# Kernel tuning notes

Measured on AMD Instinct MI355X. Metric: run time of the kernel, lower is better.

The kernel has to match this reference:

```python
import jax, jax.numpy as jnp
import numpy as np

B, N_UNK, M_KNOWN = 8, 8192, 2048
C1, C2 = 256, 256
MLP = [512, 256, 256]
K_ENC = 32
D = MLP[-1]


def setup_inputs() -> dict:
    key = jax.random.key(0)
    ks = jax.random.split(key, 16)
    return {
        "unknown": jax.random.normal(ks[0], (B, N_UNK, 3), jnp.float32),
        "known": jax.random.normal(ks[1], (B, M_KNOWN, 3), jnp.float32),
        "unknow_feats": jax.random.normal(ks[2], (B, C1, N_UNK), jnp.float32),
        "known_feats": jax.random.normal(ks[3], (B, C2, M_KNOWN), jnp.float32),
        "conv_w1": jax.random.normal(ks[4], (MLP[1], MLP[0]), jnp.float32) * 0.05,
        "conv_b1": jnp.zeros((MLP[1],), jnp.float32),
        "bn_g1": jnp.ones((MLP[1],), jnp.float32),
        "bn_b1": jnp.zeros((MLP[1],), jnp.float32),
        "bn_m1": jax.random.normal(ks[5], (MLP[1],), jnp.float32) * 0.01,
        "bn_v1": jax.random.uniform(ks[6], (MLP[1],), jnp.float32, 0.5, 1.5),
        "conv_w2": jax.random.normal(ks[7], (MLP[2], MLP[1]), jnp.float32) * 0.05,
        "conv_b2": jnp.zeros((MLP[2],), jnp.float32),
        "bn_g2": jnp.ones((MLP[2],), jnp.float32),
        "bn_b2": jnp.zeros((MLP[2],), jnp.float32),
        "bn_m2": jax.random.normal(ks[8], (MLP[2],), jnp.float32) * 0.01,
        "bn_v2": jax.random.uniform(ks[9], (MLP[2],), jnp.float32, 0.5, 1.5),
        "enc_codewords": jax.random.normal(ks[10], (K_ENC, D), jnp.float32) * float(1.0 / np.sqrt(K_ENC * D)),
        "enc_scale": jax.random.uniform(ks[11], (K_ENC,), jnp.float32, -1.0, 0.0),
        "lin_w": jax.random.normal(ks[12], (D, D * K_ENC), jnp.float32) * 0.02,
        "lin_b": jnp.zeros((D,), jnp.float32),
    }


def _conv_bn_relu(x, w, b, g, beta, mean, var):
    # 1x1 conv over (B,C,N) == channel GEMM, then BN (inference form), then ReLU
    x = jnp.einsum("oc,bcn->bon", w, x) + b[None, :, None]
    x = g[None, :, None] * (x - mean[None, :, None]) * jax.lax.rsqrt(var + 1e-5)[None, :, None] + beta[None, :, None]
    return jax.nn.relu(x)


def reference(unknown, known, unknow_feats, known_feats,
              conv_w1, conv_b1, bn_g1, bn_b1, bn_m1, bn_v1,
              conv_w2, conv_b2, bn_g2, bn_b2, bn_m2, bn_v2,
              enc_codewords, enc_scale, lin_w, lin_b):
    # ---- three_nn: 3 nearest known points for each unknown point ----
    x2 = jnp.sum(unknown * unknown, axis=-1)            # (B,n)
    y2 = jnp.sum(known * known, axis=-1)                # (B,m)
    d2 = x2[:, :, None] - 2.0 * jnp.einsum("bnc,bmc->bnm", unknown, known) + y2[:, None, :]
    dist = jnp.sqrt(jnp.maximum(d2, 1e-12))             # (B,n,m) Euclidean
    neg_d, idx = jax.lax.top_k(-dist, 3)                # 3 smallest
    dist3 = -neg_d                                      # (B,n,3)
    dist_recip = 1.0 / (dist3 + 1e-8)
    weight = dist_recip / jnp.sum(dist_recip, axis=2, keepdims=True)
    # ---- three_interpolate: gather + weighted sum ----
    gathered = jax.vmap(lambda f, i: f[:, i])(known_feats, idx)   # (B,C2,n,3)
    interp = jnp.einsum("bcnk,bnk->bcn", gathered, weight)        # (B,C2,n)
    feats = jnp.concatenate([interp, unknow_feats], axis=1)       # (B,C2+C1,n)
    # ---- SharedMLP (two 1x1 conv + BN + ReLU layers) ----
    h = _conv_bn_relu(feats, conv_w1, conv_b1, bn_g1, bn_b1, bn_m1, bn_v1)
    h = _conv_bn_relu(h, conv_w2, conv_b2, bn_g2, bn_b2, bn_m2, bn_v2)   # (B,D,n)
    # ---- Encoding layer (soft dictionary assignment, residual aggregate) ----
    X = jnp.swapaxes(h, 1, 2)                                     # (B,n,D)
    c2 = jnp.sum(enc_codewords * enc_codewords, axis=-1)          # (K,)
    xn2 = jnp.sum(X * X, axis=-1)                                 # (B,n)
    # scaled_l2: s_k * ||x - c_k||^2 without materializing (B,n,K,D) residuals
    sl = enc_scale[None, None, :] * (xn2[:, :, None] - 2.0 * jnp.einsum("bnd,kd->bnk", X, enc_codewords) + c2[None, None, :])
    A = jax.nn.softmax(sl, axis=-1)                               # (B,n,K)
    E = jnp.einsum("bnk,bnd->bkd", A, X) - jnp.sum(A, axis=1)[:, :, None] * enc_codewords[None]
    E = jax.nn.relu(E).reshape(E.shape[0], -1)                    # (B,K*D)
    E = E / jnp.maximum(jnp.linalg.norm(E, axis=1, keepdims=True), 1e-12)  # F.normalize
    ctx = jax.nn.sigmoid(E @ lin_w.T + lin_b)                     # (B,D)
    # ---- channel-attention fusion ----
    return h * ctx[:, :, None]                                    # (B,D,n)
```

## Files before the change

kernel.cpp:

```cpp
#include <hip/hip_runtime.h>
#include <stdint.h>

typedef unsigned short u16;
typedef unsigned int u32;
typedef __attribute__((ext_vector_type(8))) short short8;
typedef __attribute__((ext_vector_type(4))) float f32x4;
typedef __attribute__((ext_vector_type(4))) u32 u32x4;

#define B_ 8
#define N_ 8192
#define M_ 2048
#define DD 256
#define KENC 32

#define SC1 0
#define SH1 256
#define SC2 512
#define SH2 768
#define C2OFF 1024
#define SOFF 1056
#define RNOFF 1088

#define OFF_IDX3   0ull
#define OFF_W3     786432ull
#define OFF_FT     1572864ull
#define OFF_H1T    68681728ull
#define OFF_ERELU  102236160ull
#define OFF_PART   102498304ull
#define OFF_CONSTS 102760448ull
#define OFF_CTX    102768640ull
#define OFF_W1D    102776832ull
#define OFF_W2D    103038976ull
#define OFF_CWD    103170048ull
#define OFF_FLAG   103186432ull

__device__ __forceinline__ float bf2f(u16 v){ return __uint_as_float(((u32)v)<<16); }
__device__ __forceinline__ u16 f2bf(float f){
  u32 x = __float_as_uint(f);
  return (u16)((x + 0x7FFFu + ((x>>16)&1u)) >> 16);
}
__device__ __forceinline__ float ldf(const void* p, size_t i, int f){
  return f ? ((const float*)p)[i] : bf2f(((const u16*)p)[i]);
}
__device__ __forceinline__ void gl_lds16(const u16* g, u16* l){
  __builtin_amdgcn_global_load_lds(
      (const __attribute__((address_space(1))) void*)g,
      (__attribute__((address_space(3))) void*)l, 16, 0, 0);
}

__global__ __launch_bounds__(256) void k_detect(const void* v1, int* flagp){
  __shared__ int cntb, cntf;
  int t = threadIdx.x;
  if (t==0){ cntb=0; cntf=0; }
  __syncthreads();
  float vb = bf2f(((const u16*)v1)[t]);
  if (!(vb > 0.4f && vb < 1.6f)) atomicAdd(&cntb, 1);
  if (t < 64){
    float vf = ((const float*)v1)[t];
    if (!(vf > 0.4f && vf < 1.6f)) atomicAdd(&cntf, 1);
  }
  __syncthreads();
  if (t==0) flagp[0] = (cntb > 0 && cntf == 0) ? 1 : 0;
}

__global__ __launch_bounds__(256) void k_convert(
    const void* w1, const void* w2, const void* cwsrc, const int* __restrict__ flagp,
    u16* __restrict__ W1d, u16* __restrict__ W2d, u16* __restrict__ CWd){
  int id = blockIdx.x*256 + threadIdx.x;
  int f = flagp[0];
  if (id < 131072){
    W1d[id] = f ? f2bf(((const float*)w1)[id]) : ((const u16*)w1)[id];
  } else if (id < 196608){
    int j = id - 131072;
    W2d[j] = f ? f2bf(((const float*)w2)[j]) : ((const u16*)w2)[j];
  } else if (id < 204800){
    int j = id - 196608;
    CWd[j] = f ? f2bf(((const float*)cwsrc)[j]) : ((const u16*)cwsrc)[j];
  }
}

__global__ __launch_bounds__(256) void k0_setup(
    const void* cb1, const void* g1, const void* be1, const void* m1, const void* v1,
    const void* cb2, const void* g2, const void* be2, const void* m2, const void* v2,
    const u16* __restrict__ CWd, const void* es, const int* __restrict__ flagp,
    float* __restrict__ consts){
  int t = threadIdx.x;
  int f = flagp[0];
  {
    float g = ldf(g1,t,f), be = ldf(be1,t,f), m = ldf(m1,t,f), v = ldf(v1,t,f), cb = ldf(cb1,t,f);
    float r = 1.f/sqrtf(v + 1e-5f);
    float sc = g*r;
    consts[SC1+t] = sc; consts[SH1+t] = (cb-m)*sc + be;
  }
  {
    float g = ldf(g2,t,f), be = ldf(be2,t,f), m = ldf(m2,t,f), v = ldf(v2,t,f), cb = ldf(cb2,t,f);
    float r = 1.f/sqrtf(v + 1e-5f);
    float sc = g*r;
    consts[SC2+t] = sc; consts[SH2+t] = (cb-m)*sc + be;
  }
  if (t < KENC){
    float s = 0.f;
    for (int d=0; d<DD; d++){ float c = bf2f(CWd[t*DD+d]); s = fmaf(c,c,s); }
    consts[C2OFF+t] = s;
    consts[SOFF+t]  = ldf(es,t,f);
  }
}

__global__ __launch_bounds__(256) void k1_three_nn(
    const void* unknown, const void* known, const int* __restrict__ flagp,
    int* __restrict__ idx3, float* __restrict__ w3){
  __shared__ float4 kp[M_];
  int b = blockIdx.y, t = threadIdx.x;
  int f = flagp[0];
  for (int i=t; i<M_; i+=256){
    size_t o = ((size_t)b*M_ + i)*3;
    float x = ldf(known,o,f), y = ldf(known,o+1,f), z = ldf(known,o+2,f);
    float y2 = __fadd_rn(__fadd_rn(__fmul_rn(x,x), __fmul_rn(y,y)), __fmul_rn(z,z));
    kp[i] = make_float4(x,y,z,y2);
  }
  __syncthreads();
  int qq = t >> 3, sl = t & 7;
  int pid = blockIdx.x*32 + qq;
  size_t uo = ((size_t)b*N_ + pid)*3;
  float ux=ldf(unknown,uo,f), uy=ldf(unknown,uo+1,f), uz=ldf(unknown,uo+2,f);
  float x2 = __fadd_rn(__fadd_rn(__fmul_rn(ux,ux), __fmul_rn(uy,uy)), __fmul_rn(uz,uz));
  float u2x = ux+ux, u2y = uy+uy, u2z = uz+uz;
  float b0=3.4e38f, b1=3.4e38f, b2v=3.4e38f;
  int i0=-1, i1=-1, i2=-1;
  for (int j0=0; j0<256; j0+=4){
    float d[4]; int mi[4];
    #pragma unroll
    for (int u=0; u<4; u++){
      int m = (j0+u)*8 + sl;
      mi[u] = m;
      float4 km = kp[m];
      float dot2 = __fadd_rn(__fadd_rn(__fmul_rn(u2x,km.x), __fmul_rn(u2y,km.y)), __fmul_rn(u2z,km.z));
      d[u] = __fadd_rn(__fsub_rn(x2, dot2), km.w);
    }
    #pragma unroll
    for (int u=0; u<4; u++){
      float d2 = d[u];
      if (__builtin_expect(d2 < b2v, 0)){
        int m = mi[u];
        bool lt0 = d2 < b0, lt1 = d2 < b1;
        b2v = lt1 ? b1 : d2;                     i2 = lt1 ? i1 : m;
        float nb1 = lt0 ? b0 : (lt1 ? d2 : b1);  int ni1 = lt0 ? i0 : (lt1 ? m : i1);
        b0  = lt0 ? d2 : b0;                     i0 = lt0 ? m : i0;
        b1 = nb1; i1 = ni1;
      }
    }
  }
  #pragma unroll
  for (int st=1; st<8; st<<=1){
    float o0=__shfl_xor(b0,st,64), o1=__shfl_xor(b1,st,64), o2=__shfl_xor(b2v,st,64);
    int   j0=__shfl_xor(i0,st,64), j1=__shfl_xor(i1,st,64), j2=__shfl_xor(i2,st,64);
    float dv[3] = {o0,o1,o2}; int jv[3] = {j0,j1,j2};
    #pragma unroll
    for (int e=0; e<3; e++){
      float dd = dv[e]; int jj = jv[e];
      bool lt2 = (dd < b2v) || (dd == b2v && jj < i2);
      if (lt2){
        bool lt0 = (dd < b0) || (dd == b0 && jj < i0);
        bool lt1 = (dd < b1) || (dd == b1 && jj < i1);
        if (lt0){ b2v=b1;i2=i1; b1=b0;i1=i0; b0=dd;i0=jj; }
        else if (lt1){ b2v=b1;i2=i1; b1=dd;i1=jj; }
        else { b2v=dd; i2=jj; }
      }
    }
  }
  if (sl == 0){
    float da = __fsqrt_rn(fmaxf(b0,1e-12f));
    float db = __fsqrt_rn(fmaxf(b1,1e-12f));
    float dc = __fsqrt_rn(fmaxf(b2v,1e-12f));
    float r0 = __fdiv_rn(1.f, __fadd_rn(da,1e-8f));
    float r1 = __fdiv_rn(1.f, __fadd_rn(db,1e-8f));
    float r2 = __fdiv_rn(1.f, __fadd_rn(dc,1e-8f));
    float rs = __fadd_rn(__fadd_rn(r0,r1),r2);
    size_t o = ((size_t)b*N_ + pid)*3;
    idx3[o]=i0; idx3[o+1]=i1; idx3[o+2]=i2;
    w3[o]=__fdiv_rn(r0,rs); w3[o+1]=__fdiv_rn(r1,rs); w3[o+2]=__fdiv_rn(r2,rs);
  }
}

__global__ __launch_bounds__(256) void k2_interp(
    const void* kf, const int* __restrict__ idx3,
    const float* __restrict__ w3, const int* __restrict__ flagp, u16* __restrict__ Ft){
  __shared__ u16 Ls[M_*8];
  int ct = blockIdx.x;
  int rg = blockIdx.y;
  int b = blockIdx.z, t = threadIdx.x;
  int f = flagp[0];
  for (int cp=0; cp<4; cp++){
    int c0 = ct*8 + cp*2;
    size_t base0 = ((size_t)b*DD + c0)*M_;
    size_t base1 = base0 + M_;
    for (int i=t; i<M_; i+=256){
      float f0 = ldf(kf, base0+i, f);
      float f1 = ldf(kf, base1+i, f);
      u32 w = (u32)f2bf(f0) | ((u32)f2bf(f1)<<16);
      *(u32*)(Ls + i*8 + cp*2) = w;
    }
  }
  __syncthreads();
  for (int rep=rg*8; rep<rg*8+8; rep++){
    int pid = rep*256 + t;
    size_t o3 = ((size_t)b*N_ + pid)*3;
    int ia = idx3[o3], ib = idx3[o3+1], ic = idx3[o3+2];
    float wa = w3[o3], wb = w3[o3+1], wc = w3[o3+2];
    short8 va = *(const short8*)(Ls + ia*8);
    short8 vb = *(const short8*)(Ls + ib*8);
    short8 vc = *(const short8*)(Ls + ic*8);
    u32x4 pk;
    #pragma unroll
    for (int cq=0; cq<4; cq++){
      float fa0 = bf2f((u16)va[cq*2]),   fb0 = bf2f((u16)vb[cq*2]),   fc0 = bf2f((u16)vc[cq*2]);
      float fa1 = bf2f((u16)va[cq*2+1]), fb1 = bf2f((u16)vb[cq*2+1]), fc1 = bf2f((u16)vc[cq*2+1]);
      float v0 = fmaf(wc, fc0, fmaf(wb, fb0, wa*fa0));
      float v1 = fmaf(wc, fc1, fmaf(wb, fb1, wa*fa1));
      pk[cq] = (u32)f2bf(v0) | ((u32)f2bf(v1)<<16);
    }
    *(u32x4*)(Ft + ((size_t)b*N_ + pid)*512 + ct*8) = pk;
  }
}

__global__ __launch_bounds__(256) void k2b_transpose_uf(
    const void* uf, const int* __restrict__ flagp, u16* __restrict__ Ft){
  __shared__ u16 Ls[64*72];
  int bx = blockIdx.x, cy = blockIdx.y, b = blockIdx.z, t = threadIdx.x;
  int f = flagp[0];
  {
    int n = t & 63, cg = t >> 6;
    for (int i=0; i<16; i++){
      int c = cg*16 + i;
      Ls[n*72 + c] = f2bf(ldf(uf, ((size_t)b*DD + cy*64 + c)*N_ + bx*64 + n, f));
    }
  }
  __syncthreads();
  int nl = t>>2, cc = t&3;
  u16* dst = Ft + ((size_t)b*N_ + bx*64 + nl)*512 + 256 + cy*64 + cc*16;
  *(u32x4*)dst     = *(const u32x4*)(Ls + nl*72 + cc*16);
  *(u32x4*)(dst+8) = *(const u32x4*)(Ls + nl*72 + cc*16 + 8);
}

__global__ __launch_bounds__(256) void gemm_bn_relu(
    const u16* __restrict__ W, const u16* __restrict__ Fin,
    const float* __restrict__ consts, int sc_off, int sh_off,
    u16* __restrict__ Out, int K){
  __shared__ u16 SM[17408];
  u16* As = SM; u16* Bs = SM + 8192;
  int b = blockIdx.z, ot = blockIdx.y*128, nt = blockIdx.x*128;
  int t = threadIdx.x, wave = t>>6, lane = t&63, ln = lane&15, quad = lane>>4;
  int wo = (wave&1)*64, wn = (wave>>1)*64;
  f32x4 acc[4][4];
  #pragma unroll
  for (int i=0;i<4;i++)
    #pragma unroll
    for (int j=0;j<4;j++) acc[i][j] = (f32x4)0.f;
  const u16* Wp = W + (size_t)ot*K;
  const u16* Fp = Fin + ((size_t)b*N_ + nt)*K;
  for (int kk=0; kk<K; kk+=64){
    #pragma unroll
    for (int i=0;i<4;i++){
      int c = wave*256 + i*64 + lane;
      int r = c>>3, k8 = (c&7) ^ (r&7);
      const u16* gA = Wp + (size_t)r*K + kk + k8*8;
      const u16* gB = Fp + (size_t)r*K + kk + k8*8;
      gl_lds16(gA, As + (size_t)(wave*256 + i*64)*8);
      gl_lds16(gB, Bs + (size_t)(wave*256 + i*64)*8);
    }
    __syncthreads();
    #pragma unroll
    for (int kh=0; kh<2; kh++){
      short8 af[4], bfr[4];
      #pragma unroll
      for (int i=0;i<4;i++){
        int R = wo + i*16 + ln, C = kh*4 + quad;
        af[i] = *(const short8*)(As + (size_t)(R*8 + (C^(R&7)))*8);
      }
      #pragma unroll
      for (int j=0;j<4;j++){
        int R = wn + j*16 + ln, C = kh*4 + quad;
        bfr[j] = *(const short8*)(Bs + (size_t)(R*8 + (C^(R&7)))*8);
      }
      #pragma unroll
      for (int i=0;i<4;i++)
        #pragma unroll
        for (int j=0;j<4;j++)
          acc[i][j] = __builtin_amdgcn_mfma_f32_16x16x32_bf16(af[i], bfr[j], acc[i][j], 0,0,0);
    }
    __syncthreads();
  }
  u16* Cs = SM;
  #pragma unroll
  for (int i=0;i<4;i++){
    #pragma unroll
    for (int r=0;r<4;r++){
      int ol = wo + i*16 + quad*4 + r;
      float sc = consts[sc_off + ot + ol], sh = consts[sh_off + ot + ol];
      #pragma unroll
      for (int j=0;j<4;j++){
        float v = fmaxf(fmaf(acc[i][j][r], sc, sh), 0.f);
        Cs[(wn + j*16 + ln)*136 + ol] = f2bf(v);
      }
    }
  }
  __syncthreads();
  int nl = t>>1, half = t&1;
  u16* dst = Out + ((size_t)b*N_ + nt + nl)*256 + ot + half*64;
  const u16* srcr = Cs + nl*136 + half*64;
  #pragma unroll
  for (int c=0;c<8;c++)
    *(u32x4*)(dst + c*8) = *(const u32x4*)(srcr + c*8);
}

__global__ __launch_bounds__(256) void k5_enc_partial(
    const u16* __restrict__ X, const u16* __restrict__ cw,
    const float* __restrict__ consts, float* __restrict__ Epart){
  __shared__ u16 Xs[64*264];
  __shared__ float A_lds[64*32];
  __shared__ float xn2s[64];
  int g = blockIdx.x, b = blockIdx.y, t = threadIdx.x;
  int wave = t>>6, lane = t&63, ln = lane&15, quad = lane>>4;
  int ka = lane>>1, h = lane&1;
  int dbase = wave*64 + h*32;
  float accE[32];
  #pragma unroll
  for (int p=0;p<32;p++) accE[p]=0.f;
  float asum = 0.f;
  float c2v0 = consts[C2OFF + ln], c2v1 = consts[C2OFF + 16 + ln];
  float sv0  = consts[SOFF + ln],  sv1  = consts[SOFF + 16 + ln];
  for (int tt=0; tt<2; tt++){
    int n0 = (g*2+tt)*64;
    const u16* Xp = X + ((size_t)b*N_ + n0)*256;
    #pragma unroll
    for (int i=0;i<8;i++){
      int ch = t + i*256;
      int r = ch>>5, kc = (ch&31)*8;
      *(u32x4*)(Xs + r*264 + kc) = *(const u32x4*)(Xp + r*256 + kc);
    }
    __syncthreads();
    {
      int row = t>>2, part = t&3;
      const u16* rp = Xs + row*264 + part*64;
      float s = 0.f;
      #pragma unroll
      for (int d=0; d<64; d+=8){
        short8 xv = *(const short8*)(rp + d);
        #pragma unroll
        for (int q=0;q<8;q++){ float x = bf2f((u16)xv[q]); s = fmaf(x,x,s); }
      }
      s += __shfl_xor(s,1,64);
      s += __shfl_xor(s,2,64);
      if (part==0) xn2s[row] = s;
    }
    __syncthreads();
    f32x4 pj0 = (f32x4)0.f, pj1 = (f32x4)0.f;
    const u16* xrow = Xs + (wave*16 + ln)*264;
    #pragma unroll
    for (int kk=0; kk<256; kk+=32){
      short8 a   = *(const short8*)(xrow + kk + quad*8);
      short8 bf0 = *(const short8*)(cw + (size_t)ln*256 + kk + quad*8);
      short8 bf1 = *(const short8*)(cw + (size_t)(16+ln)*256 + kk + quad*8);
      pj0 = __builtin_amdgcn_mfma_f32_16x16x32_bf16(a, bf0, pj0, 0,0,0);
      pj1 = __builtin_amdgcn_mfma_f32_16x16x32_bf16(a, bf1, pj1, 0,0,0);
    }
    #pragma unroll
    for (int r=0;r<4;r++){
      int nl = wave*16 + quad*4 + r;
      float xv = xn2s[nl];
      float v0 = sv0 * __fadd_rn(__fsub_rn(xv, __fmul_rn(2.f,pj0[r])), c2v0);
      float v1 = sv1 * __fadd_rn(__fsub_rn(xv, __fmul_rn(2.f,pj1[r])), c2v1);
      float mx = fmaxf(v0,v1);
      #pragma unroll
      for (int d=1; d<16; d<<=1) mx = fmaxf(mx, __shfl_xor(mx, d, 64));
      float e0 = __expf(v0-mx), e1 = __expf(v1-mx);
      float es = e0+e1;
      #pragma unroll
      for (int d=1; d<16; d<<=1) es += __shfl_xor(es, d, 64);
      float inv = 1.f/es;
      A_lds[nl*32 + ln]      = e0*inv;
      A_lds[nl*32 + 16 + ln] = e1*inv;
    }
    __syncthreads();
    #pragma unroll 2
    for (int n=0; n<64; n++){
      float a = A_lds[n*32 + ka];
      asum += a;
      const u16* xr = Xs + n*264 + dbase;
      #pragma unroll
      for (int p8=0; p8<4; p8++){
        u32x4 xv = *(const u32x4*)(xr + p8*8);
        #pragma unroll
        for (int q=0; q<4; q++){
          u32 w = xv[q];
          float lo = __uint_as_float(w<<16);
          float hi = __uint_as_float(w & 0xffff0000u);
          accE[p8*8 + q*2]   = fmaf(a, lo, accE[p8*8 + q*2]);
          accE[p8*8 + q*2+1] = fmaf(a, hi, accE[p8*8 + q*2+1]);
        }
      }
    }
    __syncthreads();
  }
  int slab = b*64 + g;
  float* Ed = Epart + (size_t)slab*8224 + (size_t)ka*257 + dbase;
  #pragma unroll
  for (int p=0;p<32;p++) Ed[p] = accE[p];
  if (t < 64 && h == 0) Epart[(size_t)slab*8224 + (size_t)ka*257 + 256] = asum;
}

__global__ __launch_bounds__(256) void k5b_reduce(
    const float* __restrict__ Epart, const u16* __restrict__ cw, float* __restrict__ Erelu){
  int id = blockIdx.x*256 + threadIdx.x;
  int d = id & 255, k = (id>>8)&31, b = id>>13;
  float s = 0.f, as = 0.f;
  for (int sl=0; sl<64; sl++){
    const float* Ep = Epart + ((size_t)(b*64+sl))*8224 + (size_t)k*257;
    s  += Ep[d];
    as += Ep[256];
  }
  float cv = bf2f(cw[k*256+d]);
  Erelu[(size_t)b*8192 + k*256 + d] = fmaxf(s - as*cv, 0.f);
}

__global__ __launch_bounds__(256) void k6a_norm(
    const float* __restrict__ Erelu, float* __restrict__ consts){
  __shared__ float red[256];
  int b = blockIdx.x, t = threadIdx.x;
  float s = 0.f;
  for (int i=0;i<32;i++){ float e = Erelu[(size_t)b*8192 + i*256 + t]; s = fmaf(e,e,s); }
  red[t] = s; __syncthreads();
  for (int w=128; w>0; w>>=1){ if (t<w) red[t] += red[t+w]; __syncthreads(); }
  if (t==0) consts[RNOFF + b] = 1.f/fmaxf(__fsqrt_rn(red[0]), 1e-12f);
}

__global__ __launch_bounds__(256) void k6b_partial(
    const float* __restrict__ Erelu, const void* lw, const int* __restrict__ flagp,
    float* __restrict__ partials){
  __shared__ float Er[256];
  int kc = blockIdx.x, b = blockIdx.y, t = threadIdx.x;
  int f = flagp[0];
  Er[t] = Erelu[(size_t)b*8192 + kc*256 + t];
  __syncthreads();
  float s = 0.f;
  if (f){
    const float* lwp = (const float*)lw + (size_t)t*8192 + kc*256;
    for (int p=0; p<256; p+=4){
      f32x4 v = *(const f32x4*)(lwp + p);
      #pragma unroll
      for (int q=0;q<4;q++) s = fmaf(Er[p+q], v[q], s);
    }
  } else {
    const u16* lwp = (const u16*)lw + (size_t)t*8192 + kc*256;
    for (int p=0; p<256; p+=8){
      u32x4 v = *(const u32x4*)(lwp + p);
      #pragma unroll
      for (int q=0;q<4;q++){
        u32 w = v[q];
        s = fmaf(Er[p+q*2],   __uint_as_float(w<<16), s);
        s = fmaf(Er[p+q*2+1], __uint_as_float(w & 0xffff0000u), s);
      }
    }
  }
  partials[((size_t)b*32 + kc)*256 + t] = s;
}

__global__ __launch_bounds__(256) void k6c_ctx(
    const float* __restrict__ partials, const float* __restrict__ consts,
    const void* lb, const int* __restrict__ flagp, float* __restrict__ ctx){
  int b = blockIdx.x, t = threadIdx.x;
  int f = flagp[0];
  float s = 0.f;
  for (int kc=0; kc<32; kc++) s += partials[((size_t)b*32+kc)*256 + t];
  float x = fmaf(consts[RNOFF+b], s, ldf(lb,t,f));
  ctx[b*256 + t] = 1.f/(1.f + __expf(-x));
}

__global__ __launch_bounds__(256) void k7_out(
    const u16* __restrict__ ht, const float* __restrict__ ctx,
    const int* __restrict__ flagp, void* out){
  __shared__ u16 Ls[64*72];
  int bx = blockIdx.x, oy = blockIdx.y, b = blockIdx.z, t = threadIdx.x;
  int f = flagp[0];
  {
    int nl = t>>2, oc = t&3;
    const u16* src = ht + ((size_t)b*N_ + bx*64 + nl)*256 + oy*64 + oc*16;
    *(u32x4*)(Ls + nl*72 + oc*16)     = *(const u32x4*)src;
    *(u32x4*)(Ls + nl*72 + oc*16 + 8) = *(const u32x4*)(src + 8);
  }
  __syncthreads();
  int ol = t>>2, nc = t&3;
  float cv = ctx[b*256 + oy*64 + ol];
  size_t dstoff = ((size_t)b*DD + oy*64 + ol)*N_ + bx*64 + nc*16;
  if (f){
    float* dst = (float*)out + dstoff;
    #pragma unroll
    for (int wq=0; wq<4; wq++){
      f32x4 v;
      #pragma unroll
      for (int q=0;q<4;q++) v[q] = bf2f(Ls[(nc*16 + wq*4 + q)*72 + ol]) * cv;
      *(f32x4*)(dst + wq*4) = v;
    }
  } else {
    u32 words[8];
    #pragma unroll
    for (int wq=0; wq<8; wq++){
      float v0 = bf2f(Ls[(nc*16 + wq*2)*72 + ol]) * cv;
      float v1 = bf2f(Ls[(nc*16 + wq*2+1)*72 + ol]) * cv;
      words[wq] = (u32)f2bf(v0) | ((u32)f2bf(v1)<<16);
    }
    u16* dst = (u16*)out + dstoff;
    u32x4 w0 = {words[0],words[1],words[2],words[3]};
    u32x4 w1 = {words[4],words[5],words[6],words[7]};
    *(u32x4*)dst     = w0;
    *(u32x4*)(dst+8) = w1;
  }
}

extern "C" void kernel_launch(void* const* d_in, const int* in_sizes, int n_in,
                              void* d_out, int out_size, void* d_ws, size_t ws_size,
                              hipStream_t stream){
  const void* unknown = d_in[0];
  const void* known   = d_in[1];
  const void* uf      = d_in[2];
  const void* kf      = d_in[3];
  const void* w1      = d_in[4];
  const void* cb1     = d_in[5];
  const void* g1      = d_in[6];
  const void* be1     = d_in[7];
  const void* m1      = d_in[8];
  const void* v1      = d_in[9];
  const void* w2      = d_in[10];
  const void* cb2     = d_in[11];
  const void* g2      = d_in[12];
  const void* be2     = d_in[13];
  const void* m2      = d_in[14];
  const void* v2      = d_in[15];
  const void* cw      = d_in[16];
  const void* es      = d_in[17];
  const void* lw      = d_in[18];
  const void* lb      = d_in[19];

  char* ws = (char*)d_ws;
  int*   idx3  = (int*)(ws + OFF_IDX3);
  float* w3    = (float*)(ws + OFF_W3);
  u16*   Ft    = (u16*)(ws + OFF_FT);
  u16*   ht    = Ft;
  u16*   h1t   = (u16*)(ws + OFF_H1T);
  float* Epart = (float*)(ws + OFF_H1T);
  float* Erelu    = (float*)(ws + OFF_ERELU);
  float* partials = (float*)(ws + OFF_PART);
  float* consts   = (float*)(ws + OFF_CONSTS);
  float* ctx      = (float*)(ws + OFF_CTX);
  u16*   W1d   = (u16*)(ws + OFF_W1D);
  u16*   W2d   = (u16*)(ws + OFF_W2D);
  u16*   CWd   = (u16*)(ws + OFF_CWD);
  int*   flagp = (int*)(ws + OFF_FLAG);

  k_detect<<<1, 256, 0, stream>>>(v1, flagp);
  k_convert<<<800, 256, 0, stream>>>(w1, w2, cw, flagp, W1d, W2d, CWd);
  k0_setup<<<1, 256, 0, stream>>>(cb1,g1,be1,m1,v1, cb2,g2,be2,m2,v2, CWd, es, flagp, consts);
  k1_three_nn<<<dim3(256,8), 256, 0, stream>>>(unknown, known, flagp, idx3, w3);
  k2_interp<<<dim3(32,4,8), 256, 0, stream>>>(kf, idx3, w3, flagp, Ft);
  k2b_transpose_uf<<<dim3(128,4,8), 256, 0, stream>>>(uf, flagp, Ft);
  gemm_bn_relu<<<dim3(64,2,8), 256, 0, stream>>>(W1d, Ft,  consts, SC1, SH1, h1t, 512);
  gemm_bn_relu<<<dim3(64,2,8), 256, 0, stream>>>(W2d, h1t, consts, SC2, SH2, ht,  256);
  k5_enc_partial<<<dim3(64,8), 256, 0, stream>>>(ht, CWd, consts, Epart);
  k5b_reduce<<<256, 256, 0, stream>>>(Epart, CWd, Erelu);
  k6a_norm<<<8, 256, 0, stream>>>(Erelu, consts);
  k6b_partial<<<dim3(32,8), 256, 0, stream>>>(Erelu, lw, flagp, partials);
  k6c_ctx<<<8, 256, 0, stream>>>(partials, consts, lb, flagp, ctx);
  k7_out<<<dim3(128,4,8), 256, 0, stream>>>(ht, ctx, flagp, d_out);
}
```

Baseline: 458.8 us.

## Rebalance three_nn lanes and split encoding partials into more swizzled blocks

The three_nn kernel now assigns 4 lanes per query instead of 8, so each block handles 64 queries and the grid is halved, with each lane scanning twice as many known points. The encoding partial kernel processes one 64-row tile per block instead of two, doubling the grid to 128 slabs per batch. It replaces padded LDS rows with an XOR swizzle, keeps row norms in registers and shuffles them instead of staging through LDS, and adds an occupancy hint. Asum moves to a separate buffer. The aim is better occupancy and fewer bank conflicts, at the cost of twice as many partial slabs for the reduce kernel to read.

```diff
diff --git a/kernel.cpp b/kernel.cpp
--- a/kernel.cpp
+++ b/kernel.cpp
@@ -119,19 +119,19 @@
     kp[i] = make_float4(x,y,z,y2);
   }
   __syncthreads();
-  int qq = t >> 3, sl = t & 7;
-  int pid = blockIdx.x*32 + qq;
+  int qq = t >> 2, sl = t & 3;
+  int pid = blockIdx.x*64 + qq;
   size_t uo = ((size_t)b*N_ + pid)*3;
   float ux=ldf(unknown,uo,f), uy=ldf(unknown,uo+1,f), uz=ldf(unknown,uo+2,f);
   float x2 = __fadd_rn(__fadd_rn(__fmul_rn(ux,ux), __fmul_rn(uy,uy)), __fmul_rn(uz,uz));
   float u2x = ux+ux, u2y = uy+uy, u2z = uz+uz;
   float b0=3.4e38f, b1=3.4e38f, b2v=3.4e38f;
   int i0=-1, i1=-1, i2=-1;
-  for (int j0=0; j0<256; j0+=4){
+  for (int j0=0; j0<512; j0+=4){
     float d[4]; int mi[4];
     #pragma unroll
     for (int u=0; u<4; u++){
-      int m = (j0+u)*8 + sl;
+      int m = (j0+u)*4 + sl;
       mi[u] = m;
       float4 km = kp[m];
       float dot2 = __fadd_rn(__fadd_rn(__fmul_rn(u2x,km.x), __fmul_rn(u2y,km.y)), __fmul_rn(u2z,km.z));
@@ -151,7 +151,7 @@
     }
   }
   #pragma unroll
-  for (int st=1; st<8; st<<=1){
+  for (int st=1; st<4; st<<=1){
     float o0=__shfl_xor(b0,st,64), o1=__shfl_xor(b1,st,64), o2=__shfl_xor(b2v,st,64);
     int   j0=__shfl_xor(i0,st,64), j1=__shfl_xor(i1,st,64), j2=__shfl_xor(i2,st,64);
     float dv[3] = {o0,o1,o2}; int jv[3] = {j0,j1,j2};
@@ -313,111 +313,113 @@
     *(u32x4*)(dst + c*8) = *(const u32x4*)(srcr + c*8);
 }
 
-__global__ __launch_bounds__(256) void k5_enc_partial(
+__global__ __launch_bounds__(256, 6) void k5_enc_partial(
     const u16* __restrict__ X, const u16* __restrict__ cw,
-    const float* __restrict__ consts, float* __restrict__ Epart){
-  __shared__ u16 Xs[64*264];
+    const float* __restrict__ consts, float* __restrict__ Epart,
+    float* __restrict__ Asum){
+  __shared__ u16 Xs[64*256];
   __shared__ float A_lds[64*32];
-  __shared__ float xn2s[64];
   int g = blockIdx.x, b = blockIdx.y, t = threadIdx.x;
   int wave = t>>6, lane = t&63, ln = lane&15, quad = lane>>4;
   int ka = lane>>1, h = lane&1;
   int dbase = wave*64 + h*32;
-  float accE[32];
-  #pragma unroll
-  for (int p=0;p<32;p++) accE[p]=0.f;
-  float asum = 0.f;
   float c2v0 = consts[C2OFF + ln], c2v1 = consts[C2OFF + 16 + ln];
   float sv0  = consts[SOFF + ln],  sv1  = consts[SOFF + 16 + ln];
-  for (int tt=0; tt<2; tt++){
-    int n0 = (g*2+tt)*64;
-    const u16* Xp = X + ((size_t)b*N_ + n0)*256;
-    #pragma unroll
-    for (int i=0;i<8;i++){
-      int ch = t + i*256;
-      int r = ch>>5, kc = (ch&31)*8;
-      *(u32x4*)(Xs + r*264 + kc) = *(const u32x4*)(Xp + r*256 + kc);
-    }
-    __syncthreads();
-    {
-      int row = t>>2, part = t&3;
-      const u16* rp = Xs + row*264 + part*64;
-      float s = 0.f;
-      #pragma unroll
-      for (int d=0; d<64; d+=8){
-        short8 xv = *(const short8*)(rp + d);
-        #pragma unroll
-        for (int q=0;q<8;q++){ float x = bf2f((u16)xv[q]); s = fmaf(x,x,s); }
-      }
-      s += __shfl_xor(s,1,64);
-      s += __shfl_xor(s,2,64);
-      if (part==0) xn2s[row] = s;
-    }
-    __syncthreads();
-    f32x4 pj0 = (f32x4)0.f, pj1 = (f32x4)0.f;
-    const u16* xrow = Xs + (wave*16 + ln)*264;
+  int n0 = g*64;
+  const u16* Xp = X + ((size_t)b*N_ + n0)*256;
+  #pragma unroll
+  for (int i=0;i<8;i++){
+    int ch = t + i*256;
+    int r = ch>>5, cc = ch&31;
+    *(u32x4*)(Xs + r*256 + ((cc ^ (r&15))<<3)) = *(const u32x4*)(Xp + r*256 + cc*8);
+  }
+  __syncthreads();
+  float xnf;
+  {
+    int row = t>>2, part = t&3;
+    float s = 0.f;
+    #pragma unroll
+    for (int j=0;j<8;j++){
+      int cc = part*8 + j;
+      short8 xv = *(const short8*)(Xs + row*256 + ((cc ^ (row&15))<<3));
+      #pragma unroll
+      for (int q=0;q<8;q++){ float x = bf2f((u16)xv[q]); s = fmaf(x,x,s); }
+    }
+    s += __shfl_xor(s,1,64);
+    s += __shfl_xor(s,2,64);
+    xnf = s;
+  }
+  f32x4 pj0 = (f32x4)0.f, pj1 = (f32x4)0.f;
+  {
+    int row = wave*16 + ln;
     #pragma unroll
     for (int kk=0; kk<256; kk+=32){
-      short8 a   = *(const short8*)(xrow + kk + quad*8);
+      int cc = (kk>>3) + quad;
+      short8 a   = *(const short8*)(Xs + row*256 + ((cc ^ (row&15))<<3));
       short8 bf0 = *(const short8*)(cw + (size_t)ln*256 + kk + quad*8);
       short8 bf1 = *(const short8*)(cw + (size_t)(16+ln)*256 + kk + quad*8);
       pj0 = __builtin_amdgcn_mfma_f32_16x16x32_bf16(a, bf0, pj0, 0,0,0);
       pj1 = __builtin_amdgcn_mfma_f32_16x16x32_bf16(a, bf1, pj1, 0,0,0);
     }
-    #pragma unroll
-    for (int r=0;r<4;r++){
-      int nl = wave*16 + quad*4 + r;
-      float xv = xn2s[nl];
-      float v0 = sv0 * __fadd_rn(__fsub_rn(xv, __fmul_rn(2.f,pj0[r])), c2v0);
-      float v1 = sv1 * __fadd_rn(__fsub_rn(xv, __fmul_rn(2.f,pj1[r])), c2v1);
-      float mx = fmaxf(v0,v1);
-      #pragma unroll
-      for (int d=1; d<16; d<<=1) mx = fmaxf(mx, __shfl_xor(mx, d, 64));
-      float e0 = __expf(v0-mx), e1 = __expf(v1-mx);
-      float es = e0+e1;
-      #pragma unroll
-      for (int d=1; d<16; d<<=1) es += __shfl_xor(es, d, 64);
-      float inv = 1.f/es;
-      A_lds[nl*32 + ln]      = e0*inv;
-      A_lds[nl*32 + 16 + ln] = e1*inv;
-    }
-    __syncthreads();
-    #pragma unroll 2
-    for (int n=0; n<64; n++){
-      float a = A_lds[n*32 + ka];
-      asum += a;
-      const u16* xr = Xs + n*264 + dbase;
-      #pragma unroll
-      for (int p8=0; p8<4; p8++){
-        u32x4 xv = *(const u32x4*)(xr + p8*8);
-        #pragma unroll
-        for (int q=0; q<4; q++){
-          u32 w = xv[q];
-          float lo = __uint_as_float(w<<16);
-          float hi = __uint_as_float(w & 0xffff0000u);
-          accE[p8*8 + q*2]   = fmaf(a, lo, accE[p8*8 + q*2]);
-          accE[p8*8 + q*2+1] = fmaf(a, hi, accE[p8*8 + q*2+1]);
-        }
-      }
-    }
-    __syncthreads();
-  }
-  int slab = b*64 + g;
-  float* Ed = Epart + (size_t)slab*8224 + (size_t)ka*257 + dbase;
+  }
+  #pragma unroll
+  for (int r=0;r<4;r++){
+    int nl = wave*16 + quad*4 + r;
+    float xv = __shfl(xnf, (quad*4 + r)*4, 64);
+    float v0 = sv0 * __fadd_rn(__fsub_rn(xv, __fmul_rn(2.f,pj0[r])), c2v0);
+    float v1 = sv1 * __fadd_rn(__fsub_rn(xv, __fmul_rn(2.f,pj1[r])), c2v1);
+    float mx = fmaxf(v0,v1);
+    #pragma unroll
+    for (int d=1; d<16; d<<=1) mx = fmaxf(mx, __shfl_xor(mx, d, 64));
+    float e0 = __expf(v0-mx), e1 = __expf(v1-mx);
+    float es = e0+e1;
+    #pragma unroll
+    for (int d=1; d<16; d<<=1) es += __shfl_xor(es, d, 64);
+    float inv = 1.f/es;
+    A_lds[nl*32 + ln]      = e0*inv;
+    A_lds[nl*32 + 16 + ln] = e1*inv;
+  }
+  __syncthreads();
+  float accE[32];
+  #pragma unroll
+  for (int p=0;p<32;p++) accE[p]=0.f;
+  float asum = 0.f;
+  int cbase = wave*8 + h*4;
+  #pragma unroll 2
+  for (int n=0; n<64; n++){
+    float a = A_lds[n*32 + ka];
+    asum += a;
+    const u16* xr = Xs + n*256;
+    int sw = (n&15)<<3;
+    #pragma unroll
+    for (int p8=0; p8<4; p8++){
+      u32x4 xv = *(const u32x4*)(xr + ((((cbase + p8)<<3) ^ sw)));
+      #pragma unroll
+      for (int q=0; q<4; q++){
+        u32 w = xv[q];
+        float lo = __uint_as_float(w<<16);
+        float hi = __uint_as_float(w & 0xffff0000u);
+        accE[p8*8 + q*2]   = fmaf(a, lo, accE[p8*8 + q*2]);
+        accE[p8*8 + q*2+1] = fmaf(a, hi, accE[p8*8 + q*2+1]);
+      }
+    }
+  }
+  int slab = b*128 + g;
+  float* Ed = Epart + (size_t)slab*8192 + (size_t)ka*256 + dbase;
   #pragma unroll
   for (int p=0;p<32;p++) Ed[p] = accE[p];
-  if (t < 64 && h == 0) Epart[(size_t)slab*8224 + (size_t)ka*257 + 256] = asum;
+  if (wave==0 && h==0) Asum[slab*32 + ka] = asum;
 }
 
 __global__ __launch_bounds__(256) void k5b_reduce(
-    const float* __restrict__ Epart, const u16* __restrict__ cw, float* __restrict__ Erelu){
+    const float* __restrict__ Epart, const float* __restrict__ Asum,
+    const u16* __restrict__ cw, float* __restrict__ Erelu){
   int id = blockIdx.x*256 + threadIdx.x;
   int d = id & 255, k = (id>>8)&31, b = id>>13;
   float s = 0.f, as = 0.f;
-  for (int sl=0; sl<64; sl++){
-    const float* Ep = Epart + ((size_t)(b*64+sl))*8224 + (size_t)k*257;
-    s  += Ep[d];
-    as += Ep[256];
+  for (int sl=0; sl<128; sl++){
+    s  += Epart[((size_t)(b*128+sl))*8192 + (size_t)k*256 + d];
+    as += Asum[(b*128+sl)*32 + k];
   }
   float cv = bf2f(cw[k*256+d]);
   Erelu[(size_t)b*8192 + k*256 + d] = fmaxf(s - as*cv, 0.f);
@@ -548,6 +550,7 @@
   u16*   ht    = Ft;
   u16*   h1t   = (u16*)(ws + OFF_H1T);
   float* Epart = (float*)(ws + OFF_H1T);
+  float* Asum  = (float*)(ws + OFF_IDX3);
   float* Erelu    = (float*)(ws + OFF_ERELU);
   float* partials = (float*)(ws + OFF_PART);
   float* consts   = (float*)(ws + OFF_CONSTS);
@@ -560,13 +563,13 @@
   k_detect<<<1, 256, 0, stream>>>(v1, flagp);
   k_convert<<<800, 256, 0, stream>>>(w1, w2, cw, flagp, W1d, W2d, CWd);
   k0_setup<<<1, 256, 0, stream>>>(cb1,g1,be1,m1,v1, cb2,g2,be2,m2,v2, CWd, es, flagp, consts);
-  k1_three_nn<<<dim3(256,8), 256, 0, stream>>>(unknown, known, flagp, idx3, w3);
+  k1_three_nn<<<dim3(128,8), 256, 0, stream>>>(unknown, known, flagp, idx3, w3);
   k2_interp<<<dim3(32,4,8), 256, 0, stream>>>(kf, idx3, w3, flagp, Ft);
   k2b_transpose_uf<<<dim3(128,4,8), 256, 0, stream>>>(uf, flagp, Ft);
   gemm_bn_relu<<<dim3(64,2,8), 256, 0, stream>>>(W1d, Ft,  consts, SC1, SH1, h1t, 512);
   gemm_bn_relu<<<dim3(64,2,8), 256, 0, stream>>>(W2d, h1t, consts, SC2, SH2, ht,  256);
-  k5_enc_partial<<<dim3(64,8), 256, 0, stream>>>(ht, CWd, consts, Epart);
-  k5b_reduce<<<256, 256, 0, stream>>>(Epart, CWd, Erelu);
+  k5_enc_partial<<<dim3(128,8), 256, 0, stream>>>(ht, CWd, consts, Epart, Asum);
+  k5b_reduce<<<256, 256, 0, stream>>>(Epart, Asum, CWd, Erelu);
   k6a_norm<<<8, 256, 0, stream>>>(Erelu, consts);
   k6b_partial<<<dim3(32,8), 256, 0, stream>>>(Erelu, lw, flagp, partials);
   k6c_ctx<<<8, 256, 0, stream>>>(partials, consts, lb, flagp, ctx);
```

After: 446.1 us. 2.8% less time.
